# Optimization experiments

Hardware: AMD Instinct MI355X
Metric: run time of the kernel (lower is better)

The kernel has to match this reference:

```python
import jax, jax.numpy as jnp
import numpy as np

B, H, L, E, MODES = 32, 8, 4096, 64, 64


def setup_inputs() -> dict:
    key = jax.random.key(0)
    kx, kw, ki = jax.random.split(key, 3)
    x = jax.random.normal(kx, (B, H, L, E), dtype=jnp.float32)
    # nn.Parameter(torch.randn(E, E, modes, 2) / sqrt(E))
    weights = jax.random.normal(kw, (E, E, MODES, 2), dtype=jnp.float32) / np.sqrt(E)
    # register_buffer: sorted random permutation of [0, seq_len//2) truncated to modes (unique)
    index = jnp.sort(jax.random.permutation(ki, L // 2)[:MODES]).astype(jnp.int64)
    return {"x": x, "weights": weights, "index": index}


def reference(x, weights, index):
    # x: [B, H, L, E]
    Bs, Hs, Ls, Es = x.shape
    xt = jnp.swapaxes(x, -1, -2)                 # [B, H, E, L]
    x_ft = jnp.fft.rfft(xt, axis=-1)             # [B, H, E, L//2+1] complex64
    w_c = weights[..., 0] + 1j * weights[..., 1]  # [E, E, modes] complex
    sel = x_ft[..., index]                       # gather selected modes: [B, H, E, modes]
    out_sel = jnp.einsum('bhei,eoi->bhoi', sel, w_c)  # [B, H, E_out, modes]
    out_ft = jnp.zeros_like(x_ft).at[..., index].set(out_sel)  # scatter into zero spectrum
    y = jnp.fft.irfft(out_ft, n=Ls, axis=-1)     # [B, H, E, L]
    return jnp.swapaxes(y, -1, -2)               # [B, H, L, E]
```

## Files before the change

### kernel.cpp

```cpp
#include <hip/hip_runtime.h>
#include <hip/hip_bf16.h>
#include <math.h>

#define LTOT   4096
#define EDIM   64
#define NMODES 64
#define BH     256
#define TWO_PI 6.28318530717958647692f

typedef float f32x4 __attribute__((ext_vector_type(4)));
typedef short s16x8 __attribute__((ext_vector_type(8)));

__device__ inline unsigned short f2bf(float f) {
    unsigned u = __builtin_bit_cast(unsigned, f);
    u += 0x7fff + ((u >> 16) & 1);
    return (unsigned short)(u >> 16);
}
__device__ inline unsigned packbf(float lo, float hi) {
    float2 t; t.x = lo; t.y = hi;
    __hip_bfloat162 h = __float22bfloat162_rn(t);
    unsigned r;
    __builtin_memcpy(&r, &h, 4);
    return r;
}
__device__ inline float bf2f(unsigned lo16) {
    return __builtin_bit_cast(float, lo16 << 16);
}

__global__ void k_tab_m(const int* __restrict__ index, unsigned short* __restrict__ Tm) {
    int k = blockIdx.x;
    int f = index[k];
    for (int l = threadIdx.x; l < LTOT; l += blockDim.x) {
        int m = (f * l) & (LTOT - 1);
        float th = (float)m * (TWO_PI / (float)LTOT);
        float s, c; sincosf(th, &s, &c);
        Tm[(size_t)(2 * k) * LTOT + l]     = f2bf(c);
        Tm[(size_t)(2 * k + 1) * LTOT + l] = f2bf(-s);
    }
}
__global__ void k_tab_t(const int* __restrict__ index, unsigned short* __restrict__ Tt) {
    int l = blockIdx.x * 4 + (threadIdx.x >> 6);
    int k = threadIdx.x & 63;
    int f = index[k];
    int m = (f * l) & (LTOT - 1);
    float th = (float)m * (TWO_PI / (float)LTOT);
    float s, c; sincosf(th, &s, &c);
    ((unsigned*)Tt)[l * 64 + k] = packbf(c, s);
}
__global__ void k_wtab(const float* __restrict__ w, unsigned* __restrict__ wt) {
    int i = blockIdx.x * 256 + threadIdx.x;
    float2 v = ((const float2*)w)[i];
    wt[i] = packbf(v.x, v.y);
}

__global__ __launch_bounds__(1024, 1) void k_fused(const float* __restrict__ x,
                                                   const unsigned short* __restrict__ Tm,
                                                   const unsigned short* __restrict__ Tt,
                                                   const unsigned* __restrict__ wtab,
                                                   const int* __restrict__ index,
                                                   float* __restrict__ y) {
    int bh = blockIdx.x;
    const float* xb = x + (size_t)bh * LTOT * EDIM;

    __shared__ unsigned xT[64 * 68];
    __shared__ float    Xs[64 * 132];
    __shared__ unsigned ABl[64 * 68];

    int t = threadIdx.x;
    int lane = t & 63, w = t >> 6;
    int r = lane & 15, kb8 = lane >> 4;
    int es = w & 3, ms = w >> 2;

    int lp = t >> 4;
    int q  = t & 15;
    unsigned swzW = ((unsigned)(q & 7)) << 2;
    unsigned swzR = (((unsigned)(es & 1)) << 4) + (((unsigned)(r >> 2)) << 2);

    f32x4 acc[2]; acc[0] = (f32x4)0.f; acc[1] = (f32x4)0.f;

    float4 a0, a1;
    {
        const float* b0 = xb + (size_t)(2 * lp) * EDIM + 4 * q;
        a0 = *(const float4*)b0;
        a1 = *(const float4*)(b0 + EDIM);
    }
    for (int tile = 0; tile < 32; ++tile) {
        int l0 = tile * 128;
        {
            float A0[4] = {a0.x, a0.y, a0.z, a0.w};
            float A1[4] = {a1.x, a1.y, a1.z, a1.w};
            #pragma unroll
            for (int j = 0; j < 4; ++j) {
                int e = 4 * q + j;
                xT[e * 68 + ((unsigned)lp ^ swzW)] = packbf(A0[j], A1[j]);
            }
        }
        __syncthreads();
        if (tile + 1 < 32) {
            const float* b0 = xb + (size_t)(l0 + 128 + 2 * lp) * EDIM + 4 * q;
            a0 = *(const float4*)b0;
            a1 = *(const float4*)(b0 + EDIM);
        }
        #pragma unroll
        for (int kk = 0; kk < 4; ++kk) {
            s16x8 af = *(const s16x8*)(xT + (es * 16 + r) * 68 +
                                       (((unsigned)(kk * 16 + kb8 * 4)) ^ swzR));
            #pragma unroll
            for (int ns = 0; ns < 2; ++ns) {
                int m = ms * 32 + ns * 16 + r;
                s16x8 bf = *(const s16x8*)(Tm + (size_t)m * LTOT + l0 + kk * 32 + kb8 * 8);
                acc[ns] = __builtin_amdgcn_mfma_f32_16x16x32_bf16(af, bf, acc[ns], 0, 0, 0);
            }
        }
        __syncthreads();
    }
    #pragma unroll
    for (int ns = 0; ns < 2; ++ns)
        #pragma unroll
        for (int g = 0; g < 4; ++g)
            Xs[(es * 16 + kb8 * 4 + g) * 132 + ms * 32 + ns * 16 + r] = acc[ns][g];
    __syncthreads();

    {
        int k = lane;
        int og = w;
        int f = index[k];
        float cc = (f == 0 ? 1.0f : 2.0f) / (float)LTOT;
        float aR[4] = {}, aI[4] = {};
        for (int e = 0; e < 64; ++e) {
            float2 X = *(const float2*)&Xs[e * 132 + 2 * k];
            #pragma unroll
            for (int oi = 0; oi < 4; ++oi) {
                unsigned wv = wtab[((size_t)(e * 64 + og * 4 + oi)) * 64 + k];
                float wr = bf2f(wv & 0xffffu);
                float wi = bf2f(wv >> 16);
                aR[oi] += X.x * wr - X.y * wi;
                aI[oi] += X.x * wi + X.y * wr;
            }
        }
        #pragma unroll
        for (int oi = 0; oi < 4; ++oi) {
            int o = og * 4 + oi;
            float im = (f == 0) ? 0.0f : -cc * aI[oi];
            ABl[o * 68 + k] = packbf(cc * aR[oi], im);
        }
    }
    __syncthreads();

    s16x8 afr[4][4];
    #pragma unroll
    for (int es2 = 0; es2 < 4; ++es2)
        #pragma unroll
        for (int ks = 0; ks < 4; ++ks)
            afr[es2][ks] = *(const s16x8*)(ABl + (es2 * 16 + r) * 68 + ks * 16 + kb8 * 4);

    for (int it = 0; it < 16; ++it) {
        int ltile = w * 256 + it * 16;
        s16x8 btf[4];
        #pragma unroll
        for (int ks = 0; ks < 4; ++ks)
            btf[ks] = *(const s16x8*)(Tt + (size_t)(ltile + r) * 128 + ks * 32 + kb8 * 8);
        f32x4 oa[4];
        #pragma unroll
        for (int es2 = 0; es2 < 4; ++es2) oa[es2] = (f32x4)0.f;
        #pragma unroll
        for (int ks = 0; ks < 4; ++ks)
            #pragma unroll
            for (int es2 = 0; es2 < 4; ++es2)
                oa[es2] = __builtin_amdgcn_mfma_f32_16x16x32_bf16(afr[es2][ks], btf[ks], oa[es2], 0, 0, 0);
        float* yb = y + ((size_t)bh * LTOT + ltile + r) * EDIM;
        #pragma unroll
        for (int es2 = 0; es2 < 4; ++es2)
            *(f32x4*)(yb + es2 * 16 + kb8 * 4) = oa[es2];
    }
}

extern "C" void kernel_launch(void* const* d_in, const int* in_sizes, int n_in,
                              void* d_out, int out_size, void* d_ws, size_t ws_size,
                              hipStream_t stream) {
    const float* x     = (const float*)d_in[0];
    const float* wgt   = (const float*)d_in[1];
    const int*   index = (const int*)d_in[2];
    float* y  = (float*)d_out;
    float* ws = (float*)d_ws;

    unsigned short* Tm = (unsigned short*)ws;
    unsigned short* Tt = (unsigned short*)(ws + 262144);
    unsigned*       wt = (unsigned*)(ws + 524288);

    hipLaunchKernelGGL(k_tab_m, dim3(NMODES), dim3(256), 0, stream, index, Tm);
    hipLaunchKernelGGL(k_tab_t, dim3(1024),   dim3(256), 0, stream, index, Tt);
    hipLaunchKernelGGL(k_wtab,  dim3(1024),   dim3(256), 0, stream, wgt, wt);
    hipLaunchKernelGGL(k_fused, dim3(BH),     dim3(1024), 0, stream, x, Tm, Tt, wt, index, y);
}
```

Before: 238.5 us.

## Split fused kernel into L-partitioned forward DFT and separate mix/inverse kernel

The single 256-block fused kernel becomes two kernels. The forward DFT GEMM is split into 4 L-chunks per (b,h), giving 1024 blocks of 256 threads, with double-buffered LDS and partial spectra written to workspace. A second kernel sums the partials, does the complex mode mixing, and runs the inverse-DFT GEMM with 512 threads. The aim is better occupancy and overlap than one 1024-thread block per CU on only 256 blocks, at the cost of an extra global round trip for the partial spectra and one more launch.

```diff
diff --git a/kernel.cpp b/kernel.cpp
--- a/kernel.cpp
+++ b/kernel.cpp
@@ -53,96 +53,145 @@
     wt[i] = packbf(v.x, v.y);
 }
 
-__global__ __launch_bounds__(1024, 1) void k_fused(const float* __restrict__ x,
+__global__ __launch_bounds__(256, 4) void k_stage1(const float* __restrict__ x,
                                                    const unsigned short* __restrict__ Tm,
-                                                   const unsigned short* __restrict__ Tt,
-                                                   const unsigned* __restrict__ wtab,
-                                                   const int* __restrict__ index,
-                                                   float* __restrict__ y) {
+                                                   float* __restrict__ Xp) {
+    int bh = blockIdx.x >> 2, part = blockIdx.x & 3;
+    const float* xb = x + ((size_t)bh * LTOT + part * 1024) * EDIM;
+    __shared__ unsigned xT[2][64 * 68];
+
+    int t = threadIdx.x;
+    int q = t & 15, lp0 = t >> 4;
+    int lane = t & 63, w = t >> 6;
+    int r = lane & 15, kb8 = lane >> 4;
+    int es = w & 1, ms = w >> 1;
+    unsigned swzW = ((unsigned)(q & 7)) << 2;
+
+    f32x4 acc[2][4];
+    #pragma unroll
+    for (int i = 0; i < 2; ++i)
+        #pragma unroll
+        for (int n = 0; n < 4; ++n) acc[i][n] = (f32x4)0.f;
+
+    float4 xn[8];
+    #pragma unroll
+    for (int p = 0; p < 4; ++p) {
+        const float* b = xb + (size_t)(2 * (lp0 + p * 16)) * EDIM + 4 * q;
+        xn[2 * p]     = *(const float4*)b;
+        xn[2 * p + 1] = *(const float4*)(b + EDIM);
+    }
+    #pragma unroll
+    for (int p = 0; p < 4; ++p) {
+        float A0[4] = {xn[2*p].x, xn[2*p].y, xn[2*p].z, xn[2*p].w};
+        float A1[4] = {xn[2*p+1].x, xn[2*p+1].y, xn[2*p+1].z, xn[2*p+1].w};
+        #pragma unroll
+        for (int j = 0; j < 4; ++j)
+            xT[0][(4 * q + j) * 68 + (((unsigned)(lp0 + p * 16)) ^ swzW)] = packbf(A0[j], A1[j]);
+    }
+    __syncthreads();
+
+    for (int t8 = 0; t8 < 8; ++t8) {
+        int cur = t8 & 1;
+        if (t8 < 7) {
+            const float* tb = xb + (size_t)((t8 + 1) * 128) * EDIM;
+            #pragma unroll
+            for (int p = 0; p < 4; ++p) {
+                const float* b = tb + (size_t)(2 * (lp0 + p * 16)) * EDIM + 4 * q;
+                xn[2 * p]     = *(const float4*)b;
+                xn[2 * p + 1] = *(const float4*)(b + EDIM);
+            }
+        }
+        #pragma unroll
+        for (int kk = 0; kk < 4; ++kk) {
+            s16x8 af[2];
+            #pragma unroll
+            for (int sub = 0; sub < 2; ++sub) {
+                int row = es * 32 + sub * 16 + r;
+                unsigned swz = (((unsigned)sub) << 4) + (((unsigned)(r >> 2)) << 2);
+                af[sub] = *(const s16x8*)(xT[cur] + row * 68 + (((unsigned)(kk * 16 + kb8 * 4)) ^ swz));
+            }
+            #pragma unroll
+            for (int ns = 0; ns < 4; ++ns) {
+                int m = ms * 64 + ns * 16 + r;
+                s16x8 bf = *(const s16x8*)(Tm + (size_t)m * LTOT + part * 1024 + t8 * 128 + kk * 32 + kb8 * 8);
+                acc[0][ns] = __builtin_amdgcn_mfma_f32_16x16x32_bf16(af[0], bf, acc[0][ns], 0, 0, 0);
+                acc[1][ns] = __builtin_amdgcn_mfma_f32_16x16x32_bf16(af[1], bf, acc[1][ns], 0, 0, 0);
+            }
+        }
+        if (t8 < 7) {
+            #pragma unroll
+            for (int p = 0; p < 4; ++p) {
+                float A0[4] = {xn[2*p].x, xn[2*p].y, xn[2*p].z, xn[2*p].w};
+                float A1[4] = {xn[2*p+1].x, xn[2*p+1].y, xn[2*p+1].z, xn[2*p+1].w};
+                #pragma unroll
+                for (int j = 0; j < 4; ++j)
+                    xT[cur ^ 1][(4 * q + j) * 68 + (((unsigned)(lp0 + p * 16)) ^ swzW)] = packbf(A0[j], A1[j]);
+            }
+        }
+        __syncthreads();
+    }
+
+    float* Xb = Xp + ((size_t)part * BH + bh) * (64 * 128);
+    #pragma unroll
+    for (int sub = 0; sub < 2; ++sub)
+        #pragma unroll
+        for (int ns = 0; ns < 4; ++ns)
+            #pragma unroll
+            for (int g = 0; g < 4; ++g)
+                Xb[(es * 32 + sub * 16 + kb8 * 4 + g) * 128 + ms * 64 + ns * 16 + r] = acc[sub][ns][g];
+}
+
+__global__ __launch_bounds__(512, 4) void k_stage23(const float* __restrict__ Xp,
+                                                    const unsigned* __restrict__ wtab,
+                                                    const unsigned short* __restrict__ Tt,
+                                                    const int* __restrict__ index,
+                                                    float* __restrict__ y) {
     int bh = blockIdx.x;
-    const float* xb = x + (size_t)bh * LTOT * EDIM;
-
-    __shared__ unsigned xT[64 * 68];
-    __shared__ float    Xs[64 * 132];
+    __shared__ float XsR[64 * 68];
+    __shared__ float XsI[64 * 68];
     __shared__ unsigned ABl[64 * 68];
 
     int t = threadIdx.x;
     int lane = t & 63, w = t >> 6;
     int r = lane & 15, kb8 = lane >> 4;
-    int es = w & 3, ms = w >> 2;
-
-    int lp = t >> 4;
-    int q  = t & 15;
-    unsigned swzW = ((unsigned)(q & 7)) << 2;
-    unsigned swzR = (((unsigned)(es & 1)) << 4) + (((unsigned)(r >> 2)) << 2);
-
-    f32x4 acc[2]; acc[0] = (f32x4)0.f; acc[1] = (f32x4)0.f;
-
-    float4 a0, a1;
-    {
-        const float* b0 = xb + (size_t)(2 * lp) * EDIM + 4 * q;
-        a0 = *(const float4*)b0;
-        a1 = *(const float4*)(b0 + EDIM);
-    }
-    for (int tile = 0; tile < 32; ++tile) {
-        int l0 = tile * 128;
-        {
-            float A0[4] = {a0.x, a0.y, a0.z, a0.w};
-            float A1[4] = {a1.x, a1.y, a1.z, a1.w};
-            #pragma unroll
-            for (int j = 0; j < 4; ++j) {
-                int e = 4 * q + j;
-                xT[e * 68 + ((unsigned)lp ^ swzW)] = packbf(A0[j], A1[j]);
-            }
-        }
-        __syncthreads();
-        if (tile + 1 < 32) {
-            const float* b0 = xb + (size_t)(l0 + 128 + 2 * lp) * EDIM + 4 * q;
-            a0 = *(const float4*)b0;
-            a1 = *(const float4*)(b0 + EDIM);
-        }
-        #pragma unroll
-        for (int kk = 0; kk < 4; ++kk) {
-            s16x8 af = *(const s16x8*)(xT + (es * 16 + r) * 68 +
-                                       (((unsigned)(kk * 16 + kb8 * 4)) ^ swzR));
-            #pragma unroll
-            for (int ns = 0; ns < 2; ++ns) {
-                int m = ms * 32 + ns * 16 + r;
-                s16x8 bf = *(const s16x8*)(Tm + (size_t)m * LTOT + l0 + kk * 32 + kb8 * 8);
-                acc[ns] = __builtin_amdgcn_mfma_f32_16x16x32_bf16(af, bf, acc[ns], 0, 0, 0);
-            }
-        }
-        __syncthreads();
-    }
-    #pragma unroll
-    for (int ns = 0; ns < 2; ++ns)
-        #pragma unroll
-        for (int g = 0; g < 4; ++g)
-            Xs[(es * 16 + kb8 * 4 + g) * 132 + ms * 32 + ns * 16 + r] = acc[ns][g];
+
+    #pragma unroll
+    for (int i = 0; i < 4; ++i) {
+        int idx = t + i * 512;
+        f32x4 v = (f32x4)0.f;
+        #pragma unroll
+        for (int p = 0; p < 4; ++p)
+            v += ((const f32x4*)(Xp + ((size_t)p * BH + bh) * 8192))[idx];
+        int e = idx >> 5, k0 = (idx & 31) * 2;
+        XsR[e * 68 + k0]     = v.x;
+        XsI[e * 68 + k0]     = v.y;
+        XsR[e * 68 + k0 + 1] = v.z;
+        XsI[e * 68 + k0 + 1] = v.w;
+    }
     __syncthreads();
 
     {
         int k = lane;
-        int og = w;
         int f = index[k];
         float cc = (f == 0 ? 1.0f : 2.0f) / (float)LTOT;
-        float aR[4] = {}, aI[4] = {};
+        int o0 = w * 8;
+        float aR[8] = {}, aI[8] = {};
         for (int e = 0; e < 64; ++e) {
-            float2 X = *(const float2*)&Xs[e * 132 + 2 * k];
-            #pragma unroll
-            for (int oi = 0; oi < 4; ++oi) {
-                unsigned wv = wtab[((size_t)(e * 64 + og * 4 + oi)) * 64 + k];
+            float xr = XsR[e * 68 + k];
+            float xi = XsI[e * 68 + k];
+            #pragma unroll
+            for (int oi = 0; oi < 8; ++oi) {
+                unsigned wv = wtab[((size_t)(e * 64 + o0 + oi)) * 64 + k];
                 float wr = bf2f(wv & 0xffffu);
                 float wi = bf2f(wv >> 16);
-                aR[oi] += X.x * wr - X.y * wi;
-                aI[oi] += X.x * wi + X.y * wr;
-            }
-        }
-        #pragma unroll
-        for (int oi = 0; oi < 4; ++oi) {
-            int o = og * 4 + oi;
+                aR[oi] += xr * wr - xi * wi;
+                aI[oi] += xr * wi + xi * wr;
+            }
+        }
+        #pragma unroll
+        for (int oi = 0; oi < 8; ++oi) {
             float im = (f == 0) ? 0.0f : -cc * aI[oi];
-            ABl[o * 68 + k] = packbf(cc * aR[oi], im);
+            ABl[(o0 + oi) * 68 + k] = packbf(cc * aR[oi], im);
         }
     }
     __syncthreads();
@@ -152,10 +201,11 @@
     for (int es2 = 0; es2 < 4; ++es2)
         #pragma unroll
         for (int ks = 0; ks < 4; ++ks)
-            afr[es2][ks] = *(const s16x8*)(ABl + (es2 * 16 + r) * 68 + ks * 16 + kb8 * 4);
-
-    for (int it = 0; it < 16; ++it) {
-        int ltile = w * 256 + it * 16;
+            afr[es2][ks] = *(const s16x8*)((const unsigned short*)ABl +
+                                           (es2 * 16 + r) * 136 + ks * 32 + kb8 * 8);
+
+    for (int it = 0; it < 32; ++it) {
+        int ltile = w * 512 + it * 16;
         s16x8 btf[4];
         #pragma unroll
         for (int ks = 0; ks < 4; ++ks)
@@ -187,9 +237,11 @@
     unsigned short* Tm = (unsigned short*)ws;
     unsigned short* Tt = (unsigned short*)(ws + 262144);
     unsigned*       wt = (unsigned*)(ws + 524288);
-
-    hipLaunchKernelGGL(k_tab_m, dim3(NMODES), dim3(256), 0, stream, index, Tm);
-    hipLaunchKernelGGL(k_tab_t, dim3(1024),   dim3(256), 0, stream, index, Tt);
-    hipLaunchKernelGGL(k_wtab,  dim3(1024),   dim3(256), 0, stream, wgt, wt);
-    hipLaunchKernelGGL(k_fused, dim3(BH),     dim3(1024), 0, stream, x, Tm, Tt, wt, index, y);
-}
+    float*          Xp = ws + 786432;
+
+    hipLaunchKernelGGL(k_tab_m,   dim3(NMODES), dim3(256), 0, stream, index, Tm);
+    hipLaunchKernelGGL(k_tab_t,   dim3(1024),   dim3(256), 0, stream, index, Tt);
+    hipLaunchKernelGGL(k_wtab,    dim3(1024),   dim3(256), 0, stream, wgt, wt);
+    hipLaunchKernelGGL(k_stage1,  dim3(BH * 4), dim3(256), 0, stream, x, Tm, Xp);
+    hipLaunchKernelGGL(k_stage23, dim3(BH),     dim3(512), 0, stream, Xp, wt, Tt, index, y);
+}
```

New measurement: 220.7 us. 1.08x faster.
